# Kernel optimization log

Measured on AMD Instinct MI355X. Metric: run time of the kernel, lower is better.

## Reference

```python
import jax, jax.numpy as jnp
import numpy as np

VW, VD, VH = 96, 96, 96  # voxel_width, voxel_depth, voxel_height


def _grid_points():
    # voxel centers mapped to [-1, 1]: (2*i + 1 - N) / N
    xp = (2.0 * jnp.arange(VW) + 1.0 - VW) / VW
    yp = (2.0 * jnp.arange(VD) + 1.0 - VD) / VD
    zp = (2.0 * jnp.arange(VH) + 1.0 - VH) / VH
    X, Y, Z = jnp.meshgrid(xp, yp, zp, indexing='ij')
    return jnp.stack([X.ravel(), Y.ravel(), Z.ravel()], axis=-1)  # (V, 3)


def setup_inputs() -> dict:
    key = jax.random.key(0)
    k1, k2 = jax.random.split(key)
    B, NV, NF = 8, 2048, 512
    vertices = jax.random.uniform(k1, (B, NV, 3), dtype=jnp.float32, minval=-1.0, maxval=1.0)
    facets = jax.random.randint(k2, (B, NF, 4), 0, NV, dtype=jnp.int64)
    return {"vertices": vertices, "facets": facets}


def reference(vertices, facets):
    # vertices: (B, NV, 3) float32; facets: (B, NF, 4) int indices into vertices
    B = vertices.shape[0]
    NF = facets.shape[1]
    # vertices_to_facets: per-batch gather -> (B, NF, 4, 3)
    fverts = jax.vmap(lambda v, f: v[f])(vertices, facets)
    P = _grid_points()                      # (V, 3) voxel centers
    V = P.shape[0]

    def step(idx_map, xs):
        fi, verts = xs                      # verts: (B, 4, 3)
        v3 = verts[:, 3]                    # (B, 3)
        # T[:, j] = verts[j] - verts[3]  (columns are tetra edges)
        T = jnp.swapaxes(verts[:, :3] - v3[:, None, :], 1, 2)  # (B, 3, 3)
        a, b, c = T[:, 0, 0], T[:, 0, 1], T[:, 0, 2]
        d, e, f = T[:, 1, 0], T[:, 1, 1], T[:, 1, 2]
        g, h, i = T[:, 2, 0], T[:, 2, 1], T[:, 2, 2]
        # adjugate of T (matches t_inv_* in the original)
        adj = jnp.stack([
            jnp.stack([e * i - f * h, c * h - b * i, b * f - c * e], axis=-1),
            jnp.stack([f * g - d * i, a * i - c * g, c * d - a * f], axis=-1),
            jnp.stack([d * h - e * g, b * g - a * h, a * e - b * d], axis=-1),
        ], axis=1)                          # (B, 3, 3)
        det = a * (e * i - f * h) - b * (d * i - f * g) + c * (d * h - e * g)  # (B,)
        dvec = P[None, :, :] - v3[:, None, :]                  # (B, V, 3)
        lam = jnp.einsum('brc,bvc->bvr', adj, dvec) / det[:, None, None]  # (B, V, 3)
        lam4 = 1.0 - lam.sum(axis=-1, keepdims=True)
        lams = jnp.concatenate([lam, lam4], axis=-1)           # (B, V, 4)
        # original skips when any lambda < 0 or > 1 (strict) -> inside is inclusive
        inside = jnp.all((lams >= 0.0) & (lams <= 1.0), axis=-1)  # (B, V)
        idx_map = jnp.where((idx_map < 0) & inside, fi, idx_map)
        return idx_map, None

    idx0 = jnp.full((B, V), -1, dtype=jnp.int32)
    xs = (jnp.arange(NF, dtype=jnp.int32), jnp.swapaxes(fverts, 0, 1))
    idx_map, _ = jax.lax.scan(step, idx0, xs)
    alpha = (idx_map >= 0).astype(jnp.float32).reshape(B, VW, VD, VH)
    return alpha
```

## Files before the change

### kernel.cpp

```cpp
#include <hip/hip_runtime.h>

#pragma clang fp contract(off)

#define VWD 96
#define NVERT 2048
#define NFAC 512
#define NBATCH 8
#define NSLAB 3456
#define RECF 20
#define CULF 24

__global__ __launch_bounds__(512) void precompute_kernel(
    const float* __restrict__ vertices,
    const int*   __restrict__ facets,
    float*       __restrict__ cul,
    float*       __restrict__ body)
{
    __shared__ unsigned skey[NFAC];
    __shared__ int      sidx[NFAC];
    const int b   = blockIdx.x;
    const int tid = threadIdx.x;
    const float* vb = vertices + (size_t)b * NVERT * 3;

    for (int j = tid; j < NFAC; j += 512) {
        int4 fi = ((const int4*)facets)[b * NFAC + j];
        float x0 = vb[3*fi.x+0], y0 = vb[3*fi.x+1], z0 = vb[3*fi.x+2];
        float x1 = vb[3*fi.y+0], y1 = vb[3*fi.y+1], z1 = vb[3*fi.y+2];
        float x2 = vb[3*fi.z+0], y2 = vb[3*fi.z+1], z2 = vb[3*fi.z+2];
        float x3 = vb[3*fi.w+0], y3 = vb[3*fi.w+1], z3 = vb[3*fi.w+2];
        float a  = x0-x3, bb = x1-x3, c  = x2-x3;
        float d  = y0-y3, e  = y1-y3, f  = y2-y3;
        float g  = z0-z3, h  = z1-z3, ii = z2-z3;
        float det = a*(e*ii - f*h) - bb*(d*ii - f*g) + c*(d*h - e*g);
        skey[j] = ~__float_as_uint(fabsf(det));
        sidx[j] = j;
    }
    __syncthreads();

    for (unsigned k = 2; k <= NFAC; k <<= 1) {
        for (unsigned j = k >> 1; j > 0; j >>= 1) {
            for (int t = tid; t < NFAC; t += 512) {
                int partner = t ^ (int)j;
                if (partner > t) {
                    bool up = ((t & k) == 0);
                    unsigned ka = skey[t], kb2 = skey[partner];
                    if ((ka > kb2) == up) {
                        skey[t] = kb2; skey[partner] = ka;
                        int ia = sidx[t]; sidx[t] = sidx[partner]; sidx[partner] = ia;
                    }
                }
            }
            __syncthreads();
        }
    }

    for (int s = tid; s < NFAC; s += 512) {
        int j = sidx[s];
        int4 fi = ((const int4*)facets)[b * NFAC + j];
        float vx[4], vy[4], vz[4];
        vx[0]=vb[3*fi.x+0]; vy[0]=vb[3*fi.x+1]; vz[0]=vb[3*fi.x+2];
        vx[1]=vb[3*fi.y+0]; vy[1]=vb[3*fi.y+1]; vz[1]=vb[3*fi.y+2];
        vx[2]=vb[3*fi.z+0]; vy[2]=vb[3*fi.z+1]; vz[2]=vb[3*fi.z+2];
        vx[3]=vb[3*fi.w+0]; vy[3]=vb[3*fi.w+1]; vz[3]=vb[3*fi.w+2];
        float x0=vx[0], y0=vy[0], z0=vz[0];
        float x1=vx[1], y1=vy[1], z1=vz[1];
        float x2=vx[2], y2=vy[2], z2=vz[2];
        float x3=vx[3], y3=vy[3], z3=vz[3];
        float a  = x0-x3, bb = x1-x3, c  = x2-x3;
        float d  = y0-y3, e  = y1-y3, f  = y2-y3;
        float g  = z0-z3, h  = z1-z3, ii = z2-z3;
        float A00 = e*ii - f*h,  A01 = c*h  - bb*ii, A02 = bb*f - c*e;
        float A10 = f*g  - d*ii, A11 = a*ii - c*g,   A12 = c*d  - a*f;
        float A20 = d*h  - e*g,  A21 = bb*g - a*h,   A22 = a*e  - bb*d;
        float det = a*(e*ii - f*h) - bb*(d*ii - f*g) + c*(d*h - e*g);
        if (det < 0.0f) {
            det = -det;
            A00 = -A00; A01 = -A01; A02 = -A02;
            A10 = -A10; A11 = -A11; A12 = -A12;
            A20 = -A20; A21 = -A21; A22 = -A22;
        }
        float* cu = cul + ((size_t)b * NFAC + s) * CULF;
        cu[0] = fminf(fminf(x0,x1),fminf(x2,x3)) - 1e-4f;
        cu[1] = fminf(fminf(y0,y1),fminf(y2,y3)) - 1e-4f;
        cu[2] = fminf(fminf(z0,z1),fminf(z2,z3)) - 1e-4f;
        cu[3] = fmaxf(fmaxf(x0,x1),fmaxf(x2,x3)) + 1e-4f;
        cu[4] = fmaxf(fmaxf(y0,y1),fmaxf(y2,y3)) + 1e-4f;
        cu[5] = fmaxf(fmaxf(z0,z1),fmaxf(z2,z3)) + 1e-4f;
        const float HX = 7.0f/96.0f, HZ = 3.0f/96.0f;
        const int fa[4] = {1,0,0,0}, fbv[4] = {2,2,1,1}, fc[4] = {3,3,3,2};
        for (int p = 0; p < 4; ++p) {
            int ia = fa[p], ib = fbv[p], ic = fc[p], io = p;
            float e1x = vx[ib]-vx[ia], e1y = vy[ib]-vy[ia], e1z = vz[ib]-vz[ia];
            float e2x = vx[ic]-vx[ia], e2y = vy[ic]-vy[ia], e2z = vz[ic]-vz[ia];
            float nx = e1y*e2z - e1z*e2y;
            float ny = e1z*e2x - e1x*e2z;
            float nz = e1x*e2y - e1y*e2x;
            float sdot = nx*(vx[io]-vx[ia]) + ny*(vy[io]-vy[ia]) + nz*(vz[io]-vz[ia]);
            if (sdot > 0.0f) { nx=-nx; ny=-ny; nz=-nz; sdot=-sdot; }
            float dpl = nx*vx[ia] + ny*vy[ia] + nz*vz[ia];
            float n1s = fabsf(nx)+fabsf(ny)+fabsf(nz);
            float M = 1e-4f*(-sdot) + 1e-4f*n1s + 1e-4f;
            float rhs = dpl + M + (fabsf(nx)*HX + fabsf(ny)*HX + fabsf(nz)*HZ);
            cu[6+p*4+0] = nx; cu[6+p*4+1] = ny; cu[6+p*4+2] = nz;
            cu[6+p*4+3] = rhs;
        }
        cu[22] = 0.0f; cu[23] = 0.0f;
        const float DZ = 2.0f / 96.0f;
        float margA = det * 1e-4f + 1e-3f;
        float* bo = body + ((size_t)b * NFAC + s) * RECF;
        bo[0]  = det; bo[1]  = x3;  bo[2]  = y3;  bo[3]  = z3;
        bo[4]  = A00; bo[5]  = A01; bo[6]  = A02;
        bo[7]  = A10; bo[8]  = A11; bo[9]  = A12;
        bo[10] = A20; bo[11] = A21; bo[12] = A22;
        bo[13] = margA;
        bo[14] = det - margA;
        bo[15] = det + margA;
        float ss0 = A02 * DZ, ss1 = A12 * DZ, ss2 = A22 * DZ;
        bo[16] = ss0; bo[17] = ss1; bo[18] = ss2;
        bo[19] = ss0 + ss1 + ss2;
    }
}

__global__ __launch_bounds__(512) void mask_kernel(
    const float* __restrict__ cul,
    unsigned long long* __restrict__ masks)
{
    const int col = blockIdx.x;
    const int b   = blockIdx.y;
    const int f   = threadIdx.x;
    const int w   = threadIdx.x >> 6;
    const float* cu = cul + ((size_t)b * NFAC + f) * CULF;
    float bminx=cu[0], bminy=cu[1], bminz=cu[2];
    float bmaxx=cu[3], bmaxy=cu[4], bmaxz=cu[5];
    float n0x=cu[6],  n0y=cu[7],  n0z=cu[8],  r0=cu[9];
    float n1x=cu[10], n1y=cu[11], n1z=cu[12], r1=cu[13];
    float n2x=cu[14], n2y=cu[15], n2z=cu[16], r2=cu[17];
    float n3x=cu[18], n3y=cu[19], n3z=cu[20], r3=cu[21];

    const int sx = col / 12, sy = col % 12;
    const float cx = (float)(16*sx + 8 - VWD) / 96.0f;
    const float cy = (float)(16*sy + 8 - VWD) / 96.0f;
    const float colminx = (float)(16*sx + 1  - VWD) / 96.0f;
    const float colmaxx = (float)(16*sx + 15 - VWD) / 96.0f;
    const float colminy = (float)(16*sy + 1  - VWD) / 96.0f;
    const float colmaxy = (float)(16*sy + 15 - VWD) / 96.0f;
    const bool ovxy = (bminx <= colmaxx) & (bmaxx >= colminx) &
                      (bminy <= colmaxy) & (bmaxy >= colminy);

    const float cz0   = (float)(4 - VWD) / 96.0f;
    const float stepc = 8.0f / 96.0f;
    float d0 = n0x*cx + n0y*cy + n0z*cz0 - r0;  float s0 = n0z*stepc;
    float d1 = n1x*cx + n1y*cy + n1z*cz0 - r1;  float s1 = n1z*stepc;
    float d2 = n2x*cx + n2y*cy + n2z*cz0 - r2;  float s2 = n2z*stepc;
    float d3 = n3x*cx + n3y*cy + n3z*cz0 - r3;  float s3 = n3z*stepc;
    float zlo = (float)(1 - VWD) / 96.0f;
    float zhi = (float)(7 - VWD) / 96.0f;

    unsigned long long* mp = masks + ((size_t)b * NSLAB + (size_t)col * 24) * 8 + w;
#pragma unroll 4
    for (int sz = 0; sz < 24; ++sz) {
        bool ov = ovxy & (bminz <= zhi) & (bmaxz >= zlo) &
                  (d0 <= 0.0f) & (d1 <= 0.0f) & (d2 <= 0.0f) & (d3 <= 0.0f);
        unsigned long long bal = __ballot((int)ov);
        if ((threadIdx.x & 63) == 0) mp[(size_t)sz * 8] = bal;
        d0 += s0; d1 += s1; d2 += s2; d3 += s3;
        zlo += stepc; zhi += stepc;
    }
}

__global__ __launch_bounds__(256) void voxelize_kernel(
    const float*              __restrict__ body,
    const unsigned long long* __restrict__ masks,
    float*                    __restrict__ out)
{
    const int b    = blockIdx.y;
    const int wave = threadIdx.x >> 6;
    const int lane = threadIdx.x & 63;
    const int slab = blockIdx.x * 4 + wave;
    const int sz = slab % 24;
    const int sy = (slab / 24) % 12;
    const int sx = slab / 288;
    const int ix  = sx*8 + (lane >> 3);
    const int iy  = sy*8 + (lane & 7);
    const int iz0 = sz*4;

    const float px  = (float)(2*ix  + 1 - VWD) / 96.0f;
    const float py  = (float)(2*iy  + 1 - VWD) / 96.0f;
    const float pz0 = (float)(2*iz0 + 1 - VWD) / 96.0f;

    const unsigned long long* mp = masks + ((size_t)b * NSLAB + slab) * 8;
    const float* bb = body + (size_t)b * NFAC * RECF;

    unsigned fnd = 0u;
    for (int w = 0; w < 8; ++w) {
        unsigned long long m = mp[w];
        while (m) {
            int bit = __builtin_ctzll(m);
            m &= m - 1;
            int f = __builtin_amdgcn_readfirstlane(w * 64 + bit);
            const float* bo = bb + f * RECF;
            float det = bo[0], v3x = bo[1], v3y = bo[2], v3z = bo[3];
            float A00 = bo[4],  A01 = bo[5],  A02 = bo[6];
            float A10 = bo[7],  A11 = bo[8],  A12 = bo[9];
            float A20 = bo[10], A21 = bo[11], A22 = bo[12];
            float margA = bo[13], dhi = bo[14], mhi = bo[15];
            float ss0 = bo[16], ss1 = bo[17], ss2 = bo[18], sss = bo[19];
            float dx = px - v3x, dy = py - v3y, dz0 = pz0 - v3z;
            float n0 = A00*dx + A01*dy + A02*dz0;
            float n1 = A10*dx + A11*dy + A12*dz0;
            float n2 = A20*dx + A21*dy + A22*dz0;
            float sm = n0 + n1 + n2;
            float nmargA = -margA;
#pragma unroll
            for (int k = 0; k < 4; ++k) {
                float mn = fminf(fminf(n0, n1), n2);
                bool def = (mn >= margA) & (sm <= dhi);
                bool may = (mn >= nmargA) & (sm <= mhi);
                bool needex = may & !def & !((fnd >> k) & 1u);
                if (__any(needex)) {
                    int izk = iz0 + k;
                    float pzk = (float)(2*izk + 1 - VWD) / 96.0f;
                    float dzk = pzk - v3z;
                    float e0 = A00*dx + A01*dy + A02*dzk;
                    float e1 = A10*dx + A11*dy + A12*dzk;
                    float e2 = A20*dx + A21*dy + A22*dzk;
                    float l0 = e0 / det;
                    float l1 = e1 / det;
                    float l2 = e2 / det;
                    float l3 = 1.0f - (l0 + l1 + l2);
                    bool inside = (l0 >= 0.0f) & (l0 <= 1.0f) &
                                  (l1 >= 0.0f) & (l1 <= 1.0f) &
                                  (l2 >= 0.0f) & (l2 <= 1.0f) &
                                  (l3 >= 0.0f) & (l3 <= 1.0f);
                    if (needex & inside) fnd |= (1u << k);
                }
                if (def) fnd |= (1u << k);
                if (k < 3) { n0 += ss0; n1 += ss1; n2 += ss2; sm += sss; }
            }
            if (__all(fnd == 15u)) goto done;
        }
    }
done:
    float4 v;
    v.x = (fnd & 1u) ? 1.0f : 0.0f;
    v.y = (fnd & 2u) ? 1.0f : 0.0f;
    v.z = (fnd & 4u) ? 1.0f : 0.0f;
    v.w = (fnd & 8u) ? 1.0f : 0.0f;
    *(float4*)&out[(size_t)b*(VWD*VWD*VWD) + (size_t)ix*(VWD*VWD) + iy*VWD + iz0] = v;
}

extern "C" void kernel_launch(void* const* d_in, const int* in_sizes, int n_in,
                              void* d_out, int out_size, void* d_ws, size_t ws_size,
                              hipStream_t stream) {
    const float* vertices = (const float*)d_in[0];
    const int*   facets   = (const int*)d_in[1];
    float*       out      = (float*)d_out;

    float* cul  = (float*)d_ws;
    float* body = (float*)((char*)d_ws + (size_t)NBATCH * NFAC * CULF * 4);
    unsigned long long* msk =
        (unsigned long long*)((char*)d_ws + (size_t)NBATCH * NFAC * (CULF + RECF) * 4);

    precompute_kernel<<<NBATCH, 512, 0, stream>>>(vertices, facets, cul, body);
    mask_kernel<<<dim3(144, NBATCH), 512, 0, stream>>>(cul, msk);
    dim3 grid(NSLAB / 4, NBATCH);
    voxelize_kernel<<<grid, 256, 0, stream>>>(body, msk, out);
}
```

Measured before the change: 146.3 us.

## Replace bitonic sort with rank-by-count and prefetch next facet record

The precompute kernel drops the shared-memory bitonic sort, which needed many barriers. Each thread now works out its facet's rank by comparing its key against all 512 keys, with ties broken by index, and writes its records straight to that sorted slot. In the voxelize kernel the record for the next set mask bit is loaded while the current facet is processed, hiding scalar load latency. The prefetch holds a second record live, which uses more registers.

```diff
diff --git a/kernel.cpp b/kernel.cpp
--- a/kernel.cpp
+++ b/kernel.cpp
@@ -17,108 +17,87 @@
     float*       __restrict__ body)
 {
     __shared__ unsigned skey[NFAC];
-    __shared__ int      sidx[NFAC];
-    const int b   = blockIdx.x;
-    const int tid = threadIdx.x;
+    const int b = blockIdx.x;
+    const int j = threadIdx.x;
     const float* vb = vertices + (size_t)b * NVERT * 3;
 
-    for (int j = tid; j < NFAC; j += 512) {
-        int4 fi = ((const int4*)facets)[b * NFAC + j];
-        float x0 = vb[3*fi.x+0], y0 = vb[3*fi.x+1], z0 = vb[3*fi.x+2];
-        float x1 = vb[3*fi.y+0], y1 = vb[3*fi.y+1], z1 = vb[3*fi.y+2];
-        float x2 = vb[3*fi.z+0], y2 = vb[3*fi.z+1], z2 = vb[3*fi.z+2];
-        float x3 = vb[3*fi.w+0], y3 = vb[3*fi.w+1], z3 = vb[3*fi.w+2];
-        float a  = x0-x3, bb = x1-x3, c  = x2-x3;
-        float d  = y0-y3, e  = y1-y3, f  = y2-y3;
-        float g  = z0-z3, h  = z1-z3, ii = z2-z3;
-        float det = a*(e*ii - f*h) - bb*(d*ii - f*g) + c*(d*h - e*g);
-        skey[j] = ~__float_as_uint(fabsf(det));
-        sidx[j] = j;
-    }
+    int4 fi = ((const int4*)facets)[b * NFAC + j];
+    float vx[4], vy[4], vz[4];
+    vx[0]=vb[3*fi.x+0]; vy[0]=vb[3*fi.x+1]; vz[0]=vb[3*fi.x+2];
+    vx[1]=vb[3*fi.y+0]; vy[1]=vb[3*fi.y+1]; vz[1]=vb[3*fi.y+2];
+    vx[2]=vb[3*fi.z+0]; vy[2]=vb[3*fi.z+1]; vz[2]=vb[3*fi.z+2];
+    vx[3]=vb[3*fi.w+0]; vy[3]=vb[3*fi.w+1]; vz[3]=vb[3*fi.w+2];
+    float x0=vx[0], y0=vy[0], z0=vz[0];
+    float x1=vx[1], y1=vy[1], z1=vz[1];
+    float x2=vx[2], y2=vy[2], z2=vz[2];
+    float x3=vx[3], y3=vy[3], z3=vz[3];
+    float a  = x0-x3, bb = x1-x3, c  = x2-x3;
+    float d  = y0-y3, e  = y1-y3, f  = y2-y3;
+    float g  = z0-z3, h  = z1-z3, ii = z2-z3;
+    float A00 = e*ii - f*h,  A01 = c*h  - bb*ii, A02 = bb*f - c*e;
+    float A10 = f*g  - d*ii, A11 = a*ii - c*g,   A12 = c*d  - a*f;
+    float A20 = d*h  - e*g,  A21 = bb*g - a*h,   A22 = a*e  - bb*d;
+    float det = a*(e*ii - f*h) - bb*(d*ii - f*g) + c*(d*h - e*g);
+    if (det < 0.0f) {
+        det = -det;
+        A00 = -A00; A01 = -A01; A02 = -A02;
+        A10 = -A10; A11 = -A11; A12 = -A12;
+        A20 = -A20; A21 = -A21; A22 = -A22;
+    }
+    unsigned myk = ~__float_as_uint(det);
+    skey[j] = myk;
     __syncthreads();
 
-    for (unsigned k = 2; k <= NFAC; k <<= 1) {
-        for (unsigned j = k >> 1; j > 0; j >>= 1) {
-            for (int t = tid; t < NFAC; t += 512) {
-                int partner = t ^ (int)j;
-                if (partner > t) {
-                    bool up = ((t & k) == 0);
-                    unsigned ka = skey[t], kb2 = skey[partner];
-                    if ((ka > kb2) == up) {
-                        skey[t] = kb2; skey[partner] = ka;
-                        int ia = sidx[t]; sidx[t] = sidx[partner]; sidx[partner] = ia;
-                    }
-                }
-            }
-            __syncthreads();
-        }
-    }
-
-    for (int s = tid; s < NFAC; s += 512) {
-        int j = sidx[s];
-        int4 fi = ((const int4*)facets)[b * NFAC + j];
-        float vx[4], vy[4], vz[4];
-        vx[0]=vb[3*fi.x+0]; vy[0]=vb[3*fi.x+1]; vz[0]=vb[3*fi.x+2];
-        vx[1]=vb[3*fi.y+0]; vy[1]=vb[3*fi.y+1]; vz[1]=vb[3*fi.y+2];
-        vx[2]=vb[3*fi.z+0]; vy[2]=vb[3*fi.z+1]; vz[2]=vb[3*fi.z+2];
-        vx[3]=vb[3*fi.w+0]; vy[3]=vb[3*fi.w+1]; vz[3]=vb[3*fi.w+2];
-        float x0=vx[0], y0=vy[0], z0=vz[0];
-        float x1=vx[1], y1=vy[1], z1=vz[1];
-        float x2=vx[2], y2=vy[2], z2=vz[2];
-        float x3=vx[3], y3=vy[3], z3=vz[3];
-        float a  = x0-x3, bb = x1-x3, c  = x2-x3;
-        float d  = y0-y3, e  = y1-y3, f  = y2-y3;
-        float g  = z0-z3, h  = z1-z3, ii = z2-z3;
-        float A00 = e*ii - f*h,  A01 = c*h  - bb*ii, A02 = bb*f - c*e;
-        float A10 = f*g  - d*ii, A11 = a*ii - c*g,   A12 = c*d  - a*f;
-        float A20 = d*h  - e*g,  A21 = bb*g - a*h,   A22 = a*e  - bb*d;
-        float det = a*(e*ii - f*h) - bb*(d*ii - f*g) + c*(d*h - e*g);
-        if (det < 0.0f) {
-            det = -det;
-            A00 = -A00; A01 = -A01; A02 = -A02;
-            A10 = -A10; A11 = -A11; A12 = -A12;
-            A20 = -A20; A21 = -A21; A22 = -A22;
-        }
-        float* cu = cul + ((size_t)b * NFAC + s) * CULF;
-        cu[0] = fminf(fminf(x0,x1),fminf(x2,x3)) - 1e-4f;
-        cu[1] = fminf(fminf(y0,y1),fminf(y2,y3)) - 1e-4f;
-        cu[2] = fminf(fminf(z0,z1),fminf(z2,z3)) - 1e-4f;
-        cu[3] = fmaxf(fmaxf(x0,x1),fmaxf(x2,x3)) + 1e-4f;
-        cu[4] = fmaxf(fmaxf(y0,y1),fmaxf(y2,y3)) + 1e-4f;
-        cu[5] = fmaxf(fmaxf(z0,z1),fmaxf(z2,z3)) + 1e-4f;
-        const float HX = 7.0f/96.0f, HZ = 3.0f/96.0f;
-        const int fa[4] = {1,0,0,0}, fbv[4] = {2,2,1,1}, fc[4] = {3,3,3,2};
-        for (int p = 0; p < 4; ++p) {
-            int ia = fa[p], ib = fbv[p], ic = fc[p], io = p;
-            float e1x = vx[ib]-vx[ia], e1y = vy[ib]-vy[ia], e1z = vz[ib]-vz[ia];
-            float e2x = vx[ic]-vx[ia], e2y = vy[ic]-vy[ia], e2z = vz[ic]-vz[ia];
-            float nx = e1y*e2z - e1z*e2y;
-            float ny = e1z*e2x - e1x*e2z;
-            float nz = e1x*e2y - e1y*e2x;
-            float sdot = nx*(vx[io]-vx[ia]) + ny*(vy[io]-vy[ia]) + nz*(vz[io]-vz[ia]);
-            if (sdot > 0.0f) { nx=-nx; ny=-ny; nz=-nz; sdot=-sdot; }
-            float dpl = nx*vx[ia] + ny*vy[ia] + nz*vz[ia];
-            float n1s = fabsf(nx)+fabsf(ny)+fabsf(nz);
-            float M = 1e-4f*(-sdot) + 1e-4f*n1s + 1e-4f;
-            float rhs = dpl + M + (fabsf(nx)*HX + fabsf(ny)*HX + fabsf(nz)*HZ);
-            cu[6+p*4+0] = nx; cu[6+p*4+1] = ny; cu[6+p*4+2] = nz;
-            cu[6+p*4+3] = rhs;
-        }
-        cu[22] = 0.0f; cu[23] = 0.0f;
-        const float DZ = 2.0f / 96.0f;
-        float margA = det * 1e-4f + 1e-3f;
-        float* bo = body + ((size_t)b * NFAC + s) * RECF;
-        bo[0]  = det; bo[1]  = x3;  bo[2]  = y3;  bo[3]  = z3;
-        bo[4]  = A00; bo[5]  = A01; bo[6]  = A02;
-        bo[7]  = A10; bo[8]  = A11; bo[9]  = A12;
-        bo[10] = A20; bo[11] = A21; bo[12] = A22;
-        bo[13] = margA;
-        bo[14] = det - margA;
-        bo[15] = det + margA;
-        float ss0 = A02 * DZ, ss1 = A12 * DZ, ss2 = A22 * DZ;
-        bo[16] = ss0; bo[17] = ss1; bo[18] = ss2;
-        bo[19] = ss0 + ss1 + ss2;
-    }
+    int rank = 0;
+    const uint4* sk4 = (const uint4*)skey;
+    for (int k0 = 0; k0 < NFAC; k0 += 4) {
+        uint4 kk = sk4[k0 >> 2];
+        rank += (kk.x < myk) + ((kk.x == myk) & (k0 + 0 < j));
+        rank += (kk.y < myk) + ((kk.y == myk) & (k0 + 1 < j));
+        rank += (kk.z < myk) + ((kk.z == myk) & (k0 + 2 < j));
+        rank += (kk.w < myk) + ((kk.w == myk) & (k0 + 3 < j));
+    }
+
+    float* cu = cul + ((size_t)b * NFAC + rank) * CULF;
+    cu[0] = fminf(fminf(x0,x1),fminf(x2,x3)) - 1e-4f;
+    cu[1] = fminf(fminf(y0,y1),fminf(y2,y3)) - 1e-4f;
+    cu[2] = fminf(fminf(z0,z1),fminf(z2,z3)) - 1e-4f;
+    cu[3] = fmaxf(fmaxf(x0,x1),fmaxf(x2,x3)) + 1e-4f;
+    cu[4] = fmaxf(fmaxf(y0,y1),fmaxf(y2,y3)) + 1e-4f;
+    cu[5] = fmaxf(fmaxf(z0,z1),fmaxf(z2,z3)) + 1e-4f;
+    const float HX = 7.0f/96.0f, HZ = 3.0f/96.0f;
+    const int fa[4] = {1,0,0,0}, fbv[4] = {2,2,1,1}, fc[4] = {3,3,3,2};
+#pragma unroll
+    for (int p = 0; p < 4; ++p) {
+        int ia = fa[p], ib = fbv[p], ic = fc[p], io = p;
+        float e1x = vx[ib]-vx[ia], e1y = vy[ib]-vy[ia], e1z = vz[ib]-vz[ia];
+        float e2x = vx[ic]-vx[ia], e2y = vy[ic]-vy[ia], e2z = vz[ic]-vz[ia];
+        float nx = e1y*e2z - e1z*e2y;
+        float ny = e1z*e2x - e1x*e2z;
+        float nz = e1x*e2y - e1y*e2x;
+        float sdot = nx*(vx[io]-vx[ia]) + ny*(vy[io]-vy[ia]) + nz*(vz[io]-vz[ia]);
+        if (sdot > 0.0f) { nx=-nx; ny=-ny; nz=-nz; sdot=-sdot; }
+        float dpl = nx*vx[ia] + ny*vy[ia] + nz*vz[ia];
+        float n1s = fabsf(nx)+fabsf(ny)+fabsf(nz);
+        float M = 1e-4f*(-sdot) + 1e-4f*n1s + 1e-4f;
+        float rhs = dpl + M + (fabsf(nx)*HX + fabsf(ny)*HX + fabsf(nz)*HZ);
+        cu[6+p*4+0] = nx; cu[6+p*4+1] = ny; cu[6+p*4+2] = nz;
+        cu[6+p*4+3] = rhs;
+    }
+    cu[22] = 0.0f; cu[23] = 0.0f;
+    const float DZ = 2.0f / 96.0f;
+    float margA = det * 1e-4f + 1e-3f;
+    float* bo = body + ((size_t)b * NFAC + rank) * RECF;
+    bo[0]  = det; bo[1]  = x3;  bo[2]  = y3;  bo[3]  = z3;
+    bo[4]  = A00; bo[5]  = A01; bo[6]  = A02;
+    bo[7]  = A10; bo[8]  = A11; bo[9]  = A12;
+    bo[10] = A20; bo[11] = A21; bo[12] = A22;
+    bo[13] = margA;
+    bo[14] = det - margA;
+    bo[15] = det + margA;
+    float ss0 = A02 * DZ, ss1 = A12 * DZ, ss2 = A22 * DZ;
+    bo[16] = ss0; bo[17] = ss1; bo[18] = ss2;
+    bo[19] = ss0 + ss1 + ss2;
 }
 
 __global__ __launch_bounds__(512) void mask_kernel(
@@ -168,6 +147,23 @@
     }
 }
 
+struct Rec {
+    float det, v3x, v3y, v3z;
+    float A00, A01, A02, A10, A11, A12, A20, A21, A22;
+    float margA, dhi, mhi, ss0, ss1, ss2, sss;
+};
+
+__device__ __forceinline__ Rec loadrec(const float* __restrict__ bo) {
+    Rec r;
+    r.det = bo[0];  r.v3x = bo[1];  r.v3y = bo[2];  r.v3z = bo[3];
+    r.A00 = bo[4];  r.A01 = bo[5];  r.A02 = bo[6];
+    r.A10 = bo[7];  r.A11 = bo[8];  r.A12 = bo[9];
+    r.A20 = bo[10]; r.A21 = bo[11]; r.A22 = bo[12];
+    r.margA = bo[13]; r.dhi = bo[14]; r.mhi = bo[15];
+    r.ss0 = bo[16]; r.ss1 = bo[17]; r.ss2 = bo[18]; r.sss = bo[19];
+    return r;
+}
+
 __global__ __launch_bounds__(256) void voxelize_kernel(
     const float*              __restrict__ body,
     const unsigned long long* __restrict__ masks,
@@ -192,52 +188,62 @@
     const float* bb = body + (size_t)b * NFAC * RECF;
 
     unsigned fnd = 0u;
+
+    auto process = [&](const Rec& r) {
+        float dx = px - r.v3x, dy = py - r.v3y, dz0 = pz0 - r.v3z;
+        float n0 = r.A00*dx + r.A01*dy + r.A02*dz0;
+        float n1 = r.A10*dx + r.A11*dy + r.A12*dz0;
+        float n2 = r.A20*dx + r.A21*dy + r.A22*dz0;
+        float sm = n0 + n1 + n2;
+        float nmargA = -r.margA;
+#pragma unroll
+        for (int k = 0; k < 4; ++k) {
+            float mn = fminf(fminf(n0, n1), n2);
+            bool def = (mn >= r.margA) & (sm <= r.dhi);
+            bool may = (mn >= nmargA) & (sm <= r.mhi);
+            bool needex = may & !def & !((fnd >> k) & 1u);
+            if (__any(needex)) {
+                int izk = iz0 + k;
+                float pzk = (float)(2*izk + 1 - VWD) / 96.0f;
+                float dzk = pzk - r.v3z;
+                float e0 = r.A00*dx + r.A01*dy + r.A02*dzk;
+                float e1 = r.A10*dx + r.A11*dy + r.A12*dzk;
+                float e2 = r.A20*dx + r.A21*dy + r.A22*dzk;
+                float l0 = e0 / r.det;
+                float l1 = e1 / r.det;
+                float l2 = e2 / r.det;
+                float l3 = 1.0f - (l0 + l1 + l2);
+                bool inside = (l0 >= 0.0f) & (l0 <= 1.0f) &
+                              (l1 >= 0.0f) & (l1 <= 1.0f) &
+                              (l2 >= 0.0f) & (l2 <= 1.0f) &
+                              (l3 >= 0.0f) & (l3 <= 1.0f);
+                if (needex & inside) fnd |= (1u << k);
+            }
+            if (def) fnd |= (1u << k);
+            if (k < 3) { n0 += r.ss0; n1 += r.ss1; n2 += r.ss2; sm += r.sss; }
+        }
+    };
+
     for (int w = 0; w < 8; ++w) {
         unsigned long long m = mp[w];
-        while (m) {
-            int bit = __builtin_ctzll(m);
-            m &= m - 1;
-            int f = __builtin_amdgcn_readfirstlane(w * 64 + bit);
-            const float* bo = bb + f * RECF;
-            float det = bo[0], v3x = bo[1], v3y = bo[2], v3z = bo[3];
-            float A00 = bo[4],  A01 = bo[5],  A02 = bo[6];
-            float A10 = bo[7],  A11 = bo[8],  A12 = bo[9];
-            float A20 = bo[10], A21 = bo[11], A22 = bo[12];
-            float margA = bo[13], dhi = bo[14], mhi = bo[15];
-            float ss0 = bo[16], ss1 = bo[17], ss2 = bo[18], sss = bo[19];
-            float dx = px - v3x, dy = py - v3y, dz0 = pz0 - v3z;
-            float n0 = A00*dx + A01*dy + A02*dz0;
-            float n1 = A10*dx + A11*dy + A12*dz0;
-            float n2 = A20*dx + A21*dy + A22*dz0;
-            float sm = n0 + n1 + n2;
-            float nmargA = -margA;
-#pragma unroll
-            for (int k = 0; k < 4; ++k) {
-                float mn = fminf(fminf(n0, n1), n2);
-                bool def = (mn >= margA) & (sm <= dhi);
-                bool may = (mn >= nmargA) & (sm <= mhi);
-                bool needex = may & !def & !((fnd >> k) & 1u);
-                if (__any(needex)) {
-                    int izk = iz0 + k;
-                    float pzk = (float)(2*izk + 1 - VWD) / 96.0f;
-                    float dzk = pzk - v3z;
-                    float e0 = A00*dx + A01*dy + A02*dzk;
-                    float e1 = A10*dx + A11*dy + A12*dzk;
-                    float e2 = A20*dx + A21*dy + A22*dzk;
-                    float l0 = e0 / det;
-                    float l1 = e1 / det;
-                    float l2 = e2 / det;
-                    float l3 = 1.0f - (l0 + l1 + l2);
-                    bool inside = (l0 >= 0.0f) & (l0 <= 1.0f) &
-                                  (l1 >= 0.0f) & (l1 <= 1.0f) &
-                                  (l2 >= 0.0f) & (l2 <= 1.0f) &
-                                  (l3 >= 0.0f) & (l3 <= 1.0f);
-                    if (needex & inside) fnd |= (1u << k);
-                }
-                if (def) fnd |= (1u << k);
-                if (k < 3) { n0 += ss0; n1 += ss1; n2 += ss2; sm += sss; }
+        if (m == 0) continue;
+        int bit = __builtin_ctzll(m);
+        m &= m - 1;
+        int f = __builtin_amdgcn_readfirstlane(w * 64 + bit);
+        Rec r = loadrec(bb + f * RECF);
+        for (;;) {
+            int f2 = -1;
+            if (m) {
+                int bit2 = __builtin_ctzll(m);
+                m &= m - 1;
+                f2 = __builtin_amdgcn_readfirstlane(w * 64 + bit2);
             }
+            Rec r2;
+            if (f2 >= 0) r2 = loadrec(bb + f2 * RECF);
+            process(r);
             if (__all(fnd == 15u)) goto done;
+            if (f2 < 0) break;
+            r = r2;
         }
     }
 done:
```

Result: slower. 165.9 us (+13.3%).

## Replace bitonic sort with rank-counting scatter and SoA culling layout

Applied to the files above, without the earlier changes.

The bitonic sort over facet determinants in shared memory is replaced by each thread computing its own rank with a linear scan of all keys. The thread then scatters its precomputed record directly to that rank, which removes many barrier-separated sort stages and the second gather of vertices. The culling records move from an array-of-structures layout to a structure-of-arrays layout, so the mask kernel reads them with coalesced loads. Each thread now does a 512-key scan, and ties are broken by original index, which keeps the order stable.

```diff
diff --git a/kernel.cpp b/kernel.cpp
--- a/kernel.cpp
+++ b/kernel.cpp
@@ -8,7 +8,9 @@
 #define NBATCH 8
 #define NSLAB 3456
 #define RECF 20
-#define CULF 24
+#define CULC 22
+
+#define CUL(c, b, f) cul[(size_t)(c) * (NBATCH * NFAC) + (size_t)(b) * NFAC + (f)]
 
 __global__ __launch_bounds__(512) void precompute_kernel(
     const float* __restrict__ vertices,
@@ -17,108 +19,87 @@
     float*       __restrict__ body)
 {
     __shared__ unsigned skey[NFAC];
-    __shared__ int      sidx[NFAC];
-    const int b   = blockIdx.x;
-    const int tid = threadIdx.x;
+    const int b = blockIdx.x;
+    const int j = threadIdx.x;
     const float* vb = vertices + (size_t)b * NVERT * 3;
 
-    for (int j = tid; j < NFAC; j += 512) {
-        int4 fi = ((const int4*)facets)[b * NFAC + j];
-        float x0 = vb[3*fi.x+0], y0 = vb[3*fi.x+1], z0 = vb[3*fi.x+2];
-        float x1 = vb[3*fi.y+0], y1 = vb[3*fi.y+1], z1 = vb[3*fi.y+2];
-        float x2 = vb[3*fi.z+0], y2 = vb[3*fi.z+1], z2 = vb[3*fi.z+2];
-        float x3 = vb[3*fi.w+0], y3 = vb[3*fi.w+1], z3 = vb[3*fi.w+2];
-        float a  = x0-x3, bb = x1-x3, c  = x2-x3;
-        float d  = y0-y3, e  = y1-y3, f  = y2-y3;
-        float g  = z0-z3, h  = z1-z3, ii = z2-z3;
-        float det = a*(e*ii - f*h) - bb*(d*ii - f*g) + c*(d*h - e*g);
-        skey[j] = ~__float_as_uint(fabsf(det));
-        sidx[j] = j;
-    }
+    int4 fi = ((const int4*)facets)[b * NFAC + j];
+    float vx[4], vy[4], vz[4];
+    vx[0]=vb[3*fi.x+0]; vy[0]=vb[3*fi.x+1]; vz[0]=vb[3*fi.x+2];
+    vx[1]=vb[3*fi.y+0]; vy[1]=vb[3*fi.y+1]; vz[1]=vb[3*fi.y+2];
+    vx[2]=vb[3*fi.z+0]; vy[2]=vb[3*fi.z+1]; vz[2]=vb[3*fi.z+2];
+    vx[3]=vb[3*fi.w+0]; vy[3]=vb[3*fi.w+1]; vz[3]=vb[3*fi.w+2];
+    float x0=vx[0], y0=vy[0], z0=vz[0];
+    float x1=vx[1], y1=vy[1], z1=vz[1];
+    float x2=vx[2], y2=vy[2], z2=vz[2];
+    float x3=vx[3], y3=vy[3], z3=vz[3];
+    float a  = x0-x3, bb = x1-x3, c  = x2-x3;
+    float d  = y0-y3, e  = y1-y3, f  = y2-y3;
+    float g  = z0-z3, h  = z1-z3, ii = z2-z3;
+    float A00 = e*ii - f*h,  A01 = c*h  - bb*ii, A02 = bb*f - c*e;
+    float A10 = f*g  - d*ii, A11 = a*ii - c*g,   A12 = c*d  - a*f;
+    float A20 = d*h  - e*g,  A21 = bb*g - a*h,   A22 = a*e  - bb*d;
+    float det = a*(e*ii - f*h) - bb*(d*ii - f*g) + c*(d*h - e*g);
+    if (det < 0.0f) {
+        det = -det;
+        A00 = -A00; A01 = -A01; A02 = -A02;
+        A10 = -A10; A11 = -A11; A12 = -A12;
+        A20 = -A20; A21 = -A21; A22 = -A22;
+    }
+    unsigned myk = ~__float_as_uint(det);
+    skey[j] = myk;
     __syncthreads();
 
-    for (unsigned k = 2; k <= NFAC; k <<= 1) {
-        for (unsigned j = k >> 1; j > 0; j >>= 1) {
-            for (int t = tid; t < NFAC; t += 512) {
-                int partner = t ^ (int)j;
-                if (partner > t) {
-                    bool up = ((t & k) == 0);
-                    unsigned ka = skey[t], kb2 = skey[partner];
-                    if ((ka > kb2) == up) {
-                        skey[t] = kb2; skey[partner] = ka;
-                        int ia = sidx[t]; sidx[t] = sidx[partner]; sidx[partner] = ia;
-                    }
-                }
-            }
-            __syncthreads();
-        }
-    }
-
-    for (int s = tid; s < NFAC; s += 512) {
-        int j = sidx[s];
-        int4 fi = ((const int4*)facets)[b * NFAC + j];
-        float vx[4], vy[4], vz[4];
-        vx[0]=vb[3*fi.x+0]; vy[0]=vb[3*fi.x+1]; vz[0]=vb[3*fi.x+2];
-        vx[1]=vb[3*fi.y+0]; vy[1]=vb[3*fi.y+1]; vz[1]=vb[3*fi.y+2];
-        vx[2]=vb[3*fi.z+0]; vy[2]=vb[3*fi.z+1]; vz[2]=vb[3*fi.z+2];
-        vx[3]=vb[3*fi.w+0]; vy[3]=vb[3*fi.w+1]; vz[3]=vb[3*fi.w+2];
-        float x0=vx[0], y0=vy[0], z0=vz[0];
-        float x1=vx[1], y1=vy[1], z1=vz[1];
-        float x2=vx[2], y2=vy[2], z2=vz[2];
-        float x3=vx[3], y3=vy[3], z3=vz[3];
-        float a  = x0-x3, bb = x1-x3, c  = x2-x3;
-        float d  = y0-y3, e  = y1-y3, f  = y2-y3;
-        float g  = z0-z3, h  = z1-z3, ii = z2-z3;
-        float A00 = e*ii - f*h,  A01 = c*h  - bb*ii, A02 = bb*f - c*e;
-        float A10 = f*g  - d*ii, A11 = a*ii - c*g,   A12 = c*d  - a*f;
-        float A20 = d*h  - e*g,  A21 = bb*g - a*h,   A22 = a*e  - bb*d;
-        float det = a*(e*ii - f*h) - bb*(d*ii - f*g) + c*(d*h - e*g);
-        if (det < 0.0f) {
-            det = -det;
-            A00 = -A00; A01 = -A01; A02 = -A02;
-            A10 = -A10; A11 = -A11; A12 = -A12;
-            A20 = -A20; A21 = -A21; A22 = -A22;
-        }
-        float* cu = cul + ((size_t)b * NFAC + s) * CULF;
-        cu[0] = fminf(fminf(x0,x1),fminf(x2,x3)) - 1e-4f;
-        cu[1] = fminf(fminf(y0,y1),fminf(y2,y3)) - 1e-4f;
-        cu[2] = fminf(fminf(z0,z1),fminf(z2,z3)) - 1e-4f;
-        cu[3] = fmaxf(fmaxf(x0,x1),fmaxf(x2,x3)) + 1e-4f;
-        cu[4] = fmaxf(fmaxf(y0,y1),fmaxf(y2,y3)) + 1e-4f;
-        cu[5] = fmaxf(fmaxf(z0,z1),fmaxf(z2,z3)) + 1e-4f;
-        const float HX = 7.0f/96.0f, HZ = 3.0f/96.0f;
-        const int fa[4] = {1,0,0,0}, fbv[4] = {2,2,1,1}, fc[4] = {3,3,3,2};
-        for (int p = 0; p < 4; ++p) {
-            int ia = fa[p], ib = fbv[p], ic = fc[p], io = p;
-            float e1x = vx[ib]-vx[ia], e1y = vy[ib]-vy[ia], e1z = vz[ib]-vz[ia];
-            float e2x = vx[ic]-vx[ia], e2y = vy[ic]-vy[ia], e2z = vz[ic]-vz[ia];
-            float nx = e1y*e2z - e1z*e2y;
-            float ny = e1z*e2x - e1x*e2z;
-            float nz = e1x*e2y - e1y*e2x;
-            float sdot = nx*(vx[io]-vx[ia]) + ny*(vy[io]-vy[ia]) + nz*(vz[io]-vz[ia]);
-            if (sdot > 0.0f) { nx=-nx; ny=-ny; nz=-nz; sdot=-sdot; }
-            float dpl = nx*vx[ia] + ny*vy[ia] + nz*vz[ia];
-            float n1s = fabsf(nx)+fabsf(ny)+fabsf(nz);
-            float M = 1e-4f*(-sdot) + 1e-4f*n1s + 1e-4f;
-            float rhs = dpl + M + (fabsf(nx)*HX + fabsf(ny)*HX + fabsf(nz)*HZ);
-            cu[6+p*4+0] = nx; cu[6+p*4+1] = ny; cu[6+p*4+2] = nz;
-            cu[6+p*4+3] = rhs;
-        }
-        cu[22] = 0.0f; cu[23] = 0.0f;
-        const float DZ = 2.0f / 96.0f;
-        float margA = det * 1e-4f + 1e-3f;
-        float* bo = body + ((size_t)b * NFAC + s) * RECF;
-        bo[0]  = det; bo[1]  = x3;  bo[2]  = y3;  bo[3]  = z3;
-        bo[4]  = A00; bo[5]  = A01; bo[6]  = A02;
-        bo[7]  = A10; bo[8]  = A11; bo[9]  = A12;
-        bo[10] = A20; bo[11] = A21; bo[12] = A22;
-        bo[13] = margA;
-        bo[14] = det - margA;
-        bo[15] = det + margA;
-        float ss0 = A02 * DZ, ss1 = A12 * DZ, ss2 = A22 * DZ;
-        bo[16] = ss0; bo[17] = ss1; bo[18] = ss2;
-        bo[19] = ss0 + ss1 + ss2;
-    }
+    int rank = 0;
+    const uint4* sk4 = (const uint4*)skey;
+    for (int k0 = 0; k0 < NFAC; k0 += 4) {
+        uint4 kk = sk4[k0 >> 2];
+        rank += (kk.x < myk) + ((kk.x == myk) & (k0 + 0 < j));
+        rank += (kk.y < myk) + ((kk.y == myk) & (k0 + 1 < j));
+        rank += (kk.z < myk) + ((kk.z == myk) & (k0 + 2 < j));
+        rank += (kk.w < myk) + ((kk.w == myk) & (k0 + 3 < j));
+    }
+
+    CUL(0, b, rank) = fminf(fminf(x0,x1),fminf(x2,x3)) - 1e-4f;
+    CUL(1, b, rank) = fminf(fminf(y0,y1),fminf(y2,y3)) - 1e-4f;
+    CUL(2, b, rank) = fminf(fminf(z0,z1),fminf(z2,z3)) - 1e-4f;
+    CUL(3, b, rank) = fmaxf(fmaxf(x0,x1),fmaxf(x2,x3)) + 1e-4f;
+    CUL(4, b, rank) = fmaxf(fmaxf(y0,y1),fmaxf(y2,y3)) + 1e-4f;
+    CUL(5, b, rank) = fmaxf(fmaxf(z0,z1),fmaxf(z2,z3)) + 1e-4f;
+    const float HX = 7.0f/96.0f, HZ = 3.0f/96.0f;
+    const int fa[4] = {1,0,0,0}, fbv[4] = {2,2,1,1}, fc[4] = {3,3,3,2};
+#pragma unroll
+    for (int p = 0; p < 4; ++p) {
+        int ia = fa[p], ib = fbv[p], ic = fc[p], io = p;
+        float e1x = vx[ib]-vx[ia], e1y = vy[ib]-vy[ia], e1z = vz[ib]-vz[ia];
+        float e2x = vx[ic]-vx[ia], e2y = vy[ic]-vy[ia], e2z = vz[ic]-vz[ia];
+        float nx = e1y*e2z - e1z*e2y;
+        float ny = e1z*e2x - e1x*e2z;
+        float nz = e1x*e2y - e1y*e2x;
+        float sdot = nx*(vx[io]-vx[ia]) + ny*(vy[io]-vy[ia]) + nz*(vz[io]-vz[ia]);
+        if (sdot > 0.0f) { nx=-nx; ny=-ny; nz=-nz; sdot=-sdot; }
+        float dpl = nx*vx[ia] + ny*vy[ia] + nz*vz[ia];
+        float n1s = fabsf(nx)+fabsf(ny)+fabsf(nz);
+        float M = 1e-4f*(-sdot) + 1e-4f*n1s + 1e-4f;
+        float rhs = dpl + M + (fabsf(nx)*HX + fabsf(ny)*HX + fabsf(nz)*HZ);
+        CUL(6+p*4+0, b, rank) = nx;
+        CUL(6+p*4+1, b, rank) = ny;
+        CUL(6+p*4+2, b, rank) = nz;
+        CUL(6+p*4+3, b, rank) = rhs;
+    }
+    const float DZ = 2.0f / 96.0f;
+    float margA = det * 1e-4f + 1e-3f;
+    float* bo = body + ((size_t)b * NFAC + rank) * RECF;
+    bo[0]  = det; bo[1]  = x3;  bo[2]  = y3;  bo[3]  = z3;
+    bo[4]  = A00; bo[5]  = A01; bo[6]  = A02;
+    bo[7]  = A10; bo[8]  = A11; bo[9]  = A12;
+    bo[10] = A20; bo[11] = A21; bo[12] = A22;
+    bo[13] = margA;
+    bo[14] = det - margA;
+    bo[15] = det + margA;
+    float ss0 = A02 * DZ, ss1 = A12 * DZ, ss2 = A22 * DZ;
+    bo[16] = ss0; bo[17] = ss1; bo[18] = ss2;
+    bo[19] = ss0 + ss1 + ss2;
 }
 
 __global__ __launch_bounds__(512) void mask_kernel(
@@ -129,13 +110,12 @@
     const int b   = blockIdx.y;
     const int f   = threadIdx.x;
     const int w   = threadIdx.x >> 6;
-    const float* cu = cul + ((size_t)b * NFAC + f) * CULF;
-    float bminx=cu[0], bminy=cu[1], bminz=cu[2];
-    float bmaxx=cu[3], bmaxy=cu[4], bmaxz=cu[5];
-    float n0x=cu[6],  n0y=cu[7],  n0z=cu[8],  r0=cu[9];
-    float n1x=cu[10], n1y=cu[11], n1z=cu[12], r1=cu[13];
-    float n2x=cu[14], n2y=cu[15], n2z=cu[16], r2=cu[17];
-    float n3x=cu[18], n3y=cu[19], n3z=cu[20], r3=cu[21];
+    float bminx=CUL(0,b,f), bminy=CUL(1,b,f), bminz=CUL(2,b,f);
+    float bmaxx=CUL(3,b,f), bmaxy=CUL(4,b,f), bmaxz=CUL(5,b,f);
+    float n0x=CUL(6,b,f),  n0y=CUL(7,b,f),  n0z=CUL(8,b,f),  r0=CUL(9,b,f);
+    float n1x=CUL(10,b,f), n1y=CUL(11,b,f), n1z=CUL(12,b,f), r1=CUL(13,b,f);
+    float n2x=CUL(14,b,f), n2y=CUL(15,b,f), n2z=CUL(16,b,f), r2=CUL(17,b,f);
+    float n3x=CUL(18,b,f), n3y=CUL(19,b,f), n3z=CUL(20,b,f), r3=CUL(21,b,f);
 
     const int sx = col / 12, sy = col % 12;
     const float cx = (float)(16*sx + 8 - VWD) / 96.0f;
@@ -257,9 +237,10 @@
     float*       out      = (float*)d_out;
 
     float* cul  = (float*)d_ws;
-    float* body = (float*)((char*)d_ws + (size_t)NBATCH * NFAC * CULF * 4);
+    float* body = (float*)((char*)d_ws + (size_t)CULC * NBATCH * NFAC * 4);
     unsigned long long* msk =
-        (unsigned long long*)((char*)d_ws + (size_t)NBATCH * NFAC * (CULF + RECF) * 4);
+        (unsigned long long*)((char*)d_ws +
+                              (size_t)(CULC + RECF) * NBATCH * NFAC * 4);
 
     precompute_kernel<<<NBATCH, 512, 0, stream>>>(vertices, facets, cul, body);
     mask_kernel<<<dim3(144, NBATCH), 512, 0, stream>>>(cul, msk);
```

After: 151.2 us. 3.3% more time.
